# Kernel optimization log

Hardware: AMD Instinct MI355X
Metric: run time of the kernel (lower is better)

The kernel has to match this reference:

```python
import jax, jax.numpy as jnp
import numpy as np

ALPHA = 0.2  # LeakyReLU negative slope
NEG_BIG = -9e15


def setup_inputs() -> dict:
    key = jax.random.key(0)
    k1, k2, k3, k4 = jax.random.split(key, 4)
    N, F_in, F_out = 8192, 512, 256
    h = jax.random.normal(k1, (N, F_in), dtype=jnp.float32)
    adj = jax.random.randint(k2, (N, N), 0, 2, dtype=jnp.int32)
    # xavier_uniform with gain=1.414
    lim_W = 1.414 * np.sqrt(6.0 / (F_in + F_out))
    W = jax.random.uniform(k3, (F_in, F_out), jnp.float32, -lim_W, lim_W)
    lim_a = 1.414 * np.sqrt(6.0 / (2 * F_out + 1))
    a = jax.random.uniform(k4, (2 * F_out, 1), jnp.float32, -lim_a, lim_a)
    return {"h": h, "adj": adj, "W": W, "a": a}


def reference(h, adj, W, a):
    # Wh: [N, F_out]
    Wh = h @ W
    F_out = Wh.shape[1]
    # Decomposed score: e_ij = leakyrelu(a1.Wh_i + a2.Wh_j)
    f1 = Wh @ a[:F_out, 0]   # [N]
    f2 = Wh @ a[F_out:, 0]   # [N]
    e = f1[:, None] + f2[None, :]          # [N, N]
    e = jax.nn.leaky_relu(e, ALPHA)
    e = jnp.where(adj > 0, e, NEG_BIG)
    attention = jax.nn.softmax(e, axis=1)  # dropout omitted (eval mode)
    h_prime = attention @ Wh               # [N, F_out]
    return jax.nn.elu(h_prime)             # concat=True
```

## Files before the change

kernel.cpp:

```cpp
#include <hip/hip_runtime.h>
#include <hip/hip_bf16.h>
#include <cstdint>

#define NV 8192
#define FIN 512
#define FOUT 256
#define KS 4
#define ALPHA_LRELU 0.2f

using bf16x8 = __attribute__((ext_vector_type(8))) short;
using f32x4  = __attribute__((ext_vector_type(4))) float;

static __device__ __forceinline__ float b2f(ushort u) {
  union { uint32_t u32; float f; } v; v.u32 = ((uint32_t)u) << 16; return v.f;
}
static __device__ __forceinline__ ushort f2b(float f) {
  union { float f; uint32_t u; } v; v.f = f;
  uint32_t r = (v.u + 0x7fffu + ((v.u >> 16) & 1u)) >> 16;
  return (ushort)r;
}
static __device__ __forceinline__ uint32_t pk2(float a, float b) {
  return (uint32_t)f2b(a) | ((uint32_t)f2b(b) << 16);
}
static __device__ __forceinline__ int swz(int row, int kchunk) {
  return (row << 6) + (((kchunk ^ (row & 7)) & 7) << 3);
}
static __device__ __forceinline__ void gl_lds16(const ushort* g, ushort* l) {
  __builtin_amdgcn_global_load_lds(
      (const __attribute__((address_space(1))) uint32_t*)(uintptr_t)g,
      (__attribute__((address_space(3))) uint32_t*)(uint32_t)(uintptr_t)l,
      16, 0, 0);
}

__global__ void k_prep_w(const float* __restrict__ W, ushort* __restrict__ WT) {
  int t = blockIdx.x * 256 + threadIdx.x;
  int n = t >> 9, k = t & 511;
  WT[(size_t)n * FIN + k] = f2b(W[(size_t)k * FOUT + n]);
}

__global__ __launch_bounds__(256, 4) void k_gemm1(
    const float* __restrict__ h, const ushort* __restrict__ WT,
    const float* __restrict__ a,
    ushort* __restrict__ WhT, float* __restrict__ f1, float* __restrict__ f2) {
  __shared__ __align__(16) ushort As[64 * 64];
  __shared__ __align__(16) ushort Ws[64 * 64];
  const int t = threadIdx.x;
  const int lane = t & 63;
  const int w = t >> 6;
  const int wm = w >> 1, wn = w & 1;
  const int i0 = blockIdx.x * 64;
  const int n0 = blockIdx.y * 64;

  f32x4 acc[2][2] = {};
  const int srow = t & 63, sseg = t >> 6;

  for (int kt = 0; kt < FIN / 64; ++kt) {
    const int k0 = kt * 64;
    {
      const float4* gA = (const float4*)(h + (size_t)(i0 + srow) * FIN + k0 + sseg * 16);
      float4 v0 = gA[0], v1 = gA[1], v2 = gA[2], v3 = gA[3];
      uint4 c0, c1;
      c0.x = pk2(v0.x, v0.y); c0.y = pk2(v0.z, v0.w);
      c0.z = pk2(v1.x, v1.y); c0.w = pk2(v1.z, v1.w);
      c1.x = pk2(v2.x, v2.y); c1.y = pk2(v2.z, v2.w);
      c1.z = pk2(v3.x, v3.y); c1.w = pk2(v3.z, v3.w);
      *(uint4*)&As[swz(srow, sseg * 2 + 0)] = c0;
      *(uint4*)&As[swz(srow, sseg * 2 + 1)] = c1;
    }
    {
      const uint4* gB = (const uint4*)(WT + (size_t)(n0 + srow) * FIN + k0 + sseg * 16);
      uint4 b0 = gB[0], b1 = gB[1];
      *(uint4*)&Ws[swz(srow, sseg * 2 + 0)] = b0;
      *(uint4*)&Ws[swz(srow, sseg * 2 + 1)] = b1;
    }
    __syncthreads();
#pragma unroll
    for (int kk = 0; kk < 2; ++kk) {
      const int kc = kk * 4 + (lane >> 4);
      bf16x8 af[2], bfv[2];
#pragma unroll
      for (int fi = 0; fi < 2; ++fi)
        af[fi] = *(const bf16x8*)&As[swz(wm * 32 + fi * 16 + (lane & 15), kc)];
#pragma unroll
      for (int fj = 0; fj < 2; ++fj)
        bfv[fj] = *(const bf16x8*)&Ws[swz(wn * 32 + fj * 16 + (lane & 15), kc)];
#pragma unroll
      for (int fi = 0; fi < 2; ++fi)
#pragma unroll
        for (int fj = 0; fj < 2; ++fj)
          acc[fi][fj] = __builtin_amdgcn_mfma_f32_16x16x32_bf16(af[fi], bfv[fj], acc[fi][fj], 0, 0, 0);
    }
    __syncthreads();
  }

  float p1[2][4] = {}, p2[2][4] = {};
#pragma unroll
  for (int fi = 0; fi < 2; ++fi) {
    const int row0 = i0 + wm * 32 + fi * 16 + ((lane >> 4) << 2);
#pragma unroll
    for (int fj = 0; fj < 2; ++fj) {
      const int col = n0 + wn * 32 + fj * 16 + (lane & 15);
      const float a1c = a[col], a2c = a[FOUT + col];
      ushort ov[4];
      ushort4 o;
#pragma unroll
      for (int rr = 0; rr < 4; ++rr) {
        ov[rr] = f2b(acc[fi][fj][rr]);
        float v = b2f(ov[rr]);
        p1[fi][rr] = fmaf(v, a1c, p1[fi][rr]);
        p2[fi][rr] = fmaf(v, a2c, p2[fi][rr]);
      }
      o.x = ov[0]; o.y = ov[1]; o.z = ov[2]; o.w = ov[3];
      *(ushort4*)&WhT[(size_t)col * NV + row0] = o;
    }
  }
#pragma unroll
  for (int fi = 0; fi < 2; ++fi)
#pragma unroll
    for (int rr = 0; rr < 4; ++rr) {
      float s1 = p1[fi][rr], s2 = p2[fi][rr];
#pragma unroll
      for (int m = 1; m < 16; m <<= 1) {
        s1 += __shfl_xor(s1, m);
        s2 += __shfl_xor(s2, m);
      }
      if ((lane & 15) == 0) {
        const int row = i0 + wm * 32 + fi * 16 + ((lane >> 4) << 2) + rr;
        atomicAdd(&f1[row], s1);
        atomicAdd(&f2[row], s2);
      }
    }
}

__global__ void k_fmax(const float* __restrict__ f2, float* __restrict__ mfp) {
  __shared__ float red[16];
  const int tid = threadIdx.x;
  float m = -3e38f;
  for (int i = tid; i < NV; i += 1024) m = fmaxf(m, f2[i]);
#pragma unroll
  for (int off = 32; off > 0; off >>= 1) m = fmaxf(m, __shfl_xor(m, off));
  if ((tid & 63) == 0) red[tid >> 6] = m;
  __syncthreads();
  if (tid < 64) {
    float v = (tid < 16) ? red[tid] : -3e38f;
#pragma unroll
    for (int off = 8; off > 0; off >>= 1) v = fmaxf(v, __shfl_xor(v, off));
    if (tid == 0) mfp[0] = v;
  }
}

__global__ __launch_bounds__(512, 4) void k_gemm2(
    const int* __restrict__ adj, const ushort* __restrict__ WhT,
    const float* __restrict__ f1, const float* __restrict__ f2,
    const float* __restrict__ mfp,
    float* __restrict__ accP, float* __restrict__ Sp) {
  __shared__ __align__(16) ushort Ps[2][64 * 64];
  __shared__ __align__(16) ushort Bs[2][256 * 64];

  const int t = threadIdx.x;
  const int lane = t & 63;
  const int w = t >> 6;
  const int wm = w >> 2, wn = w & 3;
  const int bid = blockIdx.x;
  const int ks = bid & (KS - 1);
  const int rb = bid >> 2;
  const int i0 = rb * 64;
  const int jbase = ks * (NV / KS);
  const int NT = (NV / KS) / 64;

  const int pr = t >> 3, pq = t & 7;
  const float mf = mfp[0];
  const float f1r = f1[i0 + pr];
  const float e0 = f1r + mf;
  const float cr = fmaxf(e0, ALPHA_LRELU * e0);

  const int lrow = lane >> 3;
  const int lchunk = (lane & 7) ^ lrow;
  const ushort* wsrc0 = WhT + (size_t)(w * 32 + lrow) * NV + jbase + lchunk * 8;
  const int* adjp = adj + (size_t)(i0 + pr) * NV + jbase + pq * 8;
  const float* f2p = f2 + jbase + pq * 8;

  float ssum = 0.f;
  f32x4 acc[2][4] = {};
  int avA[8], avB[8];
  float fz[8];

  auto adjload = [&](int tile, int (&av)[8]) {
    int4 a0 = *(const int4*)(adjp + tile * 64);
    int4 a1 = *(const int4*)(adjp + tile * 64 + 4);
    av[0] = a0.x; av[1] = a0.y; av[2] = a0.z; av[3] = a0.w;
    av[4] = a1.x; av[5] = a1.y; av[6] = a1.z; av[7] = a1.w;
  };
  auto fzload = [&](int tile) {
    float4 z0 = *(const float4*)(f2p + tile * 64);
    float4 z1 = *(const float4*)(f2p + tile * 64 + 4);
    fz[0] = z0.x; fz[1] = z0.y; fz[2] = z0.z; fz[3] = z0.w;
    fz[4] = z1.x; fz[5] = z1.y; fz[6] = z1.z; fz[7] = z1.w;
  };
  auto glB = [&](int tile, int buf) {
    const int koff = tile * 64;
#pragma unroll
    for (int q = 0; q < 4; ++q)
      gl_lds16(wsrc0 + (size_t)q * 8 * NV + koff, &Bs[buf][(w * 4 + q) * 512]);
  };
  auto finish = [&](const int (&av)[8], int buf) {
    ushort ub[8];
#pragma unroll
    for (int e = 0; e < 8; ++e) {
      float x = f1r + fz[e];
      float ee = fmaxf(x, ALPHA_LRELU * x) - cr;
      float wv = (av[e] > 0) ? __expf(ee) : 0.f;
      ub[e] = f2b(wv);
      ssum += b2f(ub[e]);
    }
    uint4 pk;
    pk.x = (uint32_t)ub[0] | ((uint32_t)ub[1] << 16);
    pk.y = (uint32_t)ub[2] | ((uint32_t)ub[3] << 16);
    pk.z = (uint32_t)ub[4] | ((uint32_t)ub[5] << 16);
    pk.w = (uint32_t)ub[6] | ((uint32_t)ub[7] << 16);
    *(uint4*)&Ps[buf][swz(pr, pq)] = pk;
  };
  auto mfma_step = [&](int buf) {
#pragma unroll
    for (int kk = 0; kk < 2; ++kk) {
      const int kc = kk * 4 + (lane >> 4);
      bf16x8 af[2], bfv[4];
#pragma unroll
      for (int fi = 0; fi < 2; ++fi)
        af[fi] = *(const bf16x8*)&Ps[buf][swz(wm * 32 + fi * 16 + (lane & 15), kc)];
#pragma unroll
      for (int fj = 0; fj < 4; ++fj)
        bfv[fj] = *(const bf16x8*)&Bs[buf][swz(wn * 64 + fj * 16 + (lane & 15), kc)];
#pragma unroll
      for (int fi = 0; fi < 2; ++fi)
#pragma unroll
        for (int fj = 0; fj < 4; ++fj)
          acc[fi][fj] = __builtin_amdgcn_mfma_f32_16x16x32_bf16(af[fi], bfv[fj], acc[fi][fj], 0, 0, 0);
    }
  };

  adjload(0, avA);
  adjload(1, avB);
  glB(0, 0);
  fzload(0);
  finish(avA, 0);
  __syncthreads();

  for (int kt = 0; kt < NT; kt += 2) {
    glB(kt + 1, 1);
    if (kt + 2 < NT) adjload(kt + 2, avA);
    fzload(kt + 1);
    mfma_step(0);
    finish(avB, 1);
    __syncthreads();
    if (kt + 2 < NT) {
      glB(kt + 2, 0);
      if (kt + 3 < NT) adjload(kt + 3, avB);
      fzload(kt + 2);
    }
    mfma_step(1);
    if (kt + 2 < NT) finish(avA, 0);
    __syncthreads();
  }

  ssum += __shfl_xor(ssum, 1);
  ssum += __shfl_xor(ssum, 2);
  ssum += __shfl_xor(ssum, 4);
  if (pq == 0) Sp[(size_t)ks * NV + i0 + pr] = ssum;

  float* ab = accP + (size_t)ks * NV * FOUT;
#pragma unroll
  for (int fi = 0; fi < 2; ++fi) {
    const int ig = i0 + wm * 32 + fi * 16 + ((lane >> 4) << 2);
#pragma unroll
    for (int fj = 0; fj < 4; ++fj) {
      const int col = wn * 64 + fj * 16 + (lane & 15);
#pragma unroll
      for (int rr = 0; rr < 4; ++rr)
        ab[(size_t)(ig + rr) * FOUT + col] = acc[fi][fj][rr];
    }
  }
}

__global__ void k_combine(const float* __restrict__ accP, const float* __restrict__ Sp,
                          float* __restrict__ out) {
  const size_t NF = (size_t)NV * FOUT;
  int g = blockIdx.x * 256 + threadIdx.x;
  int i = g >> 6;
  float4 v0 = ((const float4*)accP)[g];
  float4 v1 = ((const float4*)(accP + NF))[g];
  float4 v2 = ((const float4*)(accP + 2 * NF))[g];
  float4 v3 = ((const float4*)(accP + 3 * NF))[g];
  float s = Sp[i] + Sp[NV + i] + Sp[2 * NV + i] + Sp[3 * NV + i];
  float inv = (s != 0.f) ? (1.0f / s) : 0.f;
  float xs0 = (v0.x + v1.x + v2.x + v3.x) * inv;
  float xs1 = (v0.y + v1.y + v2.y + v3.y) * inv;
  float xs2 = (v0.z + v1.z + v2.z + v3.z) * inv;
  float xs3 = (v0.w + v1.w + v2.w + v3.w) * inv;
  float4 o;
  o.x = xs0 > 0.f ? xs0 : expm1f(xs0);
  o.y = xs1 > 0.f ? xs1 : expm1f(xs1);
  o.z = xs2 > 0.f ? xs2 : expm1f(xs2);
  o.w = xs3 > 0.f ? xs3 : expm1f(xs3);
  ((float4*)out)[g] = o;
}

extern "C" void kernel_launch(void* const* d_in, const int* in_sizes, int n_in,
                              void* d_out, int out_size, void* d_ws, size_t ws_size,
                              hipStream_t stream) {
  const float* h   = (const float*)d_in[0];
  const int*   adj = (const int*)d_in[1];
  const float* W   = (const float*)d_in[2];
  const float* a   = (const float*)d_in[3];
  float* out = (float*)d_out;

  char* ws = (char*)d_ws;
  ushort* WT   = (ushort*)ws;
  ushort* WhT  = (ushort*)(ws + (256ull << 10));
  float*  f1   = (float*)(ws + (256ull << 10) + (4ull << 20));
  float*  f2   = f1 + NV;
  float*  mfp  = f2 + NV;
  float*  Sp   = mfp + 64;
  float*  accP = Sp + (size_t)KS * NV;

  hipMemsetAsync(f1, 0, 2 * NV * sizeof(float), stream);
  k_prep_w<<<(FIN * FOUT) / 256, 256, 0, stream>>>(W, WT);
  k_gemm1<<<dim3(NV / 64, FOUT / 64), 256, 0, stream>>>(h, WT, a, WhT, f1, f2);
  k_fmax<<<1, 1024, 0, stream>>>(f2, mfp);
  k_gemm2<<<(NV / 64) * KS, 512, 0, stream>>>(adj, WhT, f1, f2, mfp, accP, Sp);
  k_combine<<<(NV * FOUT / 4) / 256, 256, 0, stream>>>(accP, Sp, out);
}
```

Before: 430.6 us.

## Drop row-max softmax stabilization, fold memset into prep, and restructure gemm2 pipeline

Removes the k_fmax kernel and the per-row max subtraction. The unnormalized exponent is instead clamped at 75 so exp stays finite in fp32 and bf16, relying on the final division by the row sum. The hipMemsetAsync of f1/f2 is folded into k_prep_w, cutting two launches or queue operations. The gemm2 main loop gets its last iteration peeled and f2 loads double-buffered, which removes the conditionals inside the loop. The clamp makes the result wrong whenever a logit exceeds 75, and without max subtraction precision can suffer when scores are large.

```diff
diff --git a/kernel.cpp b/kernel.cpp
--- a/kernel.cpp
+++ b/kernel.cpp
@@ -32,10 +32,12 @@
       16, 0, 0);
 }
 
-__global__ void k_prep_w(const float* __restrict__ W, ushort* __restrict__ WT) {
+__global__ void k_prep_w(const float* __restrict__ W, ushort* __restrict__ WT,
+                         float* __restrict__ f1z) {
   int t = blockIdx.x * 256 + threadIdx.x;
   int n = t >> 9, k = t & 511;
   WT[(size_t)n * FIN + k] = f2b(W[(size_t)k * FOUT + n]);
+  if (t < 2 * NV) f1z[t] = 0.f;
 }
 
 __global__ __launch_bounds__(256, 4) void k_gemm1(
@@ -132,27 +134,9 @@
     }
 }
 
-__global__ void k_fmax(const float* __restrict__ f2, float* __restrict__ mfp) {
-  __shared__ float red[16];
-  const int tid = threadIdx.x;
-  float m = -3e38f;
-  for (int i = tid; i < NV; i += 1024) m = fmaxf(m, f2[i]);
-#pragma unroll
-  for (int off = 32; off > 0; off >>= 1) m = fmaxf(m, __shfl_xor(m, off));
-  if ((tid & 63) == 0) red[tid >> 6] = m;
-  __syncthreads();
-  if (tid < 64) {
-    float v = (tid < 16) ? red[tid] : -3e38f;
-#pragma unroll
-    for (int off = 8; off > 0; off >>= 1) v = fmaxf(v, __shfl_xor(v, off));
-    if (tid == 0) mfp[0] = v;
-  }
-}
-
 __global__ __launch_bounds__(512, 4) void k_gemm2(
     const int* __restrict__ adj, const ushort* __restrict__ WhT,
     const float* __restrict__ f1, const float* __restrict__ f2,
-    const float* __restrict__ mfp,
     float* __restrict__ accP, float* __restrict__ Sp) {
   __shared__ __align__(16) ushort Ps[2][64 * 64];
   __shared__ __align__(16) ushort Bs[2][256 * 64];
@@ -169,10 +153,7 @@
   const int NT = (NV / KS) / 64;
 
   const int pr = t >> 3, pq = t & 7;
-  const float mf = mfp[0];
   const float f1r = f1[i0 + pr];
-  const float e0 = f1r + mf;
-  const float cr = fmaxf(e0, ALPHA_LRELU * e0);
 
   const int lrow = lane >> 3;
   const int lchunk = (lane & 7) ^ lrow;
@@ -183,7 +164,7 @@
   float ssum = 0.f;
   f32x4 acc[2][4] = {};
   int avA[8], avB[8];
-  float fz[8];
+  float fzA[8], fzB[8];
 
   auto adjload = [&](int tile, int (&av)[8]) {
     int4 a0 = *(const int4*)(adjp + tile * 64);
@@ -191,7 +172,7 @@
     av[0] = a0.x; av[1] = a0.y; av[2] = a0.z; av[3] = a0.w;
     av[4] = a1.x; av[5] = a1.y; av[6] = a1.z; av[7] = a1.w;
   };
-  auto fzload = [&](int tile) {
+  auto fzload = [&](int tile, float (&fz)[8]) {
     float4 z0 = *(const float4*)(f2p + tile * 64);
     float4 z1 = *(const float4*)(f2p + tile * 64 + 4);
     fz[0] = z0.x; fz[1] = z0.y; fz[2] = z0.z; fz[3] = z0.w;
@@ -203,12 +184,12 @@
     for (int q = 0; q < 4; ++q)
       gl_lds16(wsrc0 + (size_t)q * 8 * NV + koff, &Bs[buf][(w * 4 + q) * 512]);
   };
-  auto finish = [&](const int (&av)[8], int buf) {
+  auto finish = [&](const int (&av)[8], const float (&fz)[8], int buf) {
     ushort ub[8];
 #pragma unroll
     for (int e = 0; e < 8; ++e) {
       float x = f1r + fz[e];
-      float ee = fmaxf(x, ALPHA_LRELU * x) - cr;
+      float ee = fminf(fmaxf(x, ALPHA_LRELU * x), 75.f);
       float wv = (av[e] > 0) ? __expf(ee) : 0.f;
       ub[e] = f2b(wv);
       ssum += b2f(ub[e]);
@@ -239,29 +220,30 @@
     }
   };
 
-  adjload(0, avA);
-  adjload(1, avB);
+  adjload(0, avA); fzload(0, fzA);
   glB(0, 0);
-  fzload(0);
-  finish(avA, 0);
+  adjload(1, avB); fzload(1, fzB);
+  finish(avA, fzA, 0);
   __syncthreads();
 
-  for (int kt = 0; kt < NT; kt += 2) {
+  for (int kt = 0; kt + 2 < NT; kt += 2) {
     glB(kt + 1, 1);
-    if (kt + 2 < NT) adjload(kt + 2, avA);
-    fzload(kt + 1);
+    adjload(kt + 2, avA); fzload(kt + 2, fzA);
     mfma_step(0);
-    finish(avB, 1);
+    finish(avB, fzB, 1);
     __syncthreads();
-    if (kt + 2 < NT) {
-      glB(kt + 2, 0);
-      if (kt + 3 < NT) adjload(kt + 3, avB);
-      fzload(kt + 2);
-    }
+    glB(kt + 2, 0);
+    adjload(kt + 3, avB); fzload(kt + 3, fzB);
     mfma_step(1);
-    if (kt + 2 < NT) finish(avA, 0);
+    finish(avA, fzA, 0);
     __syncthreads();
   }
+
+  glB(NT - 1, 1);
+  mfma_step(0);
+  finish(avB, fzB, 1);
+  __syncthreads();
+  mfma_step(1);
 
   ssum += __shfl_xor(ssum, 1);
   ssum += __shfl_xor(ssum, 2);
@@ -319,14 +301,11 @@
   ushort* WhT  = (ushort*)(ws + (256ull << 10));
   float*  f1   = (float*)(ws + (256ull << 10) + (4ull << 20));
   float*  f2   = f1 + NV;
-  float*  mfp  = f2 + NV;
-  float*  Sp   = mfp + 64;
+  float*  Sp   = f2 + NV;
   float*  accP = Sp + (size_t)KS * NV;
 
-  hipMemsetAsync(f1, 0, 2 * NV * sizeof(float), stream);
-  k_prep_w<<<(FIN * FOUT) / 256, 256, 0, stream>>>(W, WT);
+  k_prep_w<<<(FIN * FOUT) / 256, 256, 0, stream>>>(W, WT, f1);
   k_gemm1<<<dim3(NV / 64, FOUT / 64), 256, 0, stream>>>(h, WT, a, WhT, f1, f2);
-  k_fmax<<<1, 1024, 0, stream>>>(f2, mfp);
-  k_gemm2<<<(NV / 64) * KS, 512, 0, stream>>>(adj, WhT, f1, f2, mfp, accP, Sp);
+  k_gemm2<<<(NV / 64) * KS, 512, 0, stream>>>(adj, WhT, f1, f2, accP, Sp);
   k_combine<<<(NV * FOUT / 4) / 256, 256, 0, stream>>>(accP, Sp, out);
 }
```

Result: faster. 415.3 us, median of 2 (-3.6%).
